# Optimization experiments

Hardware: AMD Instinct MI355X
Metric: run time of the kernel (lower is better)

Reference implementation:

```python
import jax, jax.numpy as jnp
import numpy as np

N, E, IN_F, H, F = 4096, 131072, 512, 8, 32  # n_nodes, n_edges, in_features, n_heads, n_hidden
SLOPE = 0.2


def setup_inputs() -> dict:
    key = jax.random.key(0)
    k1, k2, k3, k4 = jax.random.split(key, 4)
    h = jax.random.normal(k1, (N, IN_F), dtype=jnp.float32)
    edge_index = jax.random.randint(k2, (2, E), 0, N)
    train_mask = jnp.ones((E + N,), dtype=jnp.float32)  # mask values written into adj (incl. self-loops appended in forward)
    W_fc = jax.random.normal(k3, (IN_F, H * F), dtype=jnp.float32) * (1.0 / np.sqrt(IN_F))
    W_attn = jax.random.normal(k4, (2 * F,), dtype=jnp.float32) * (1.0 / np.sqrt(2 * F))
    return {"h": h, "edge_index": edge_index, "train_mask": train_mask, "W_fc": W_fc, "W_attn": W_attn}


def reference(h, edge_index, train_mask, W_fc, W_attn):
    n = h.shape[0]
    g = (h @ W_fc).reshape(n, H, F)  # [n, H, F]
    # attn_fc(concat(g_i, g_j)) == g_i @ W_attn[:F] + g_j @ W_attn[F:]  (same math, no NxNx2F tensor)
    el = g @ W_attn[:F]  # [n, H], contribution of source row i
    er = g @ W_attn[F:]  # [n, H], contribution of column j
    e = jax.nn.leaky_relu(el[:, None, :] + er[None, :, :], SLOPE)  # [n, n, H]
    # adjacency: edges (+ self-loops appended in forward) get train_mask values, then diagonal forced to 1
    src = jnp.concatenate([edge_index[0], jnp.arange(n)])
    dst = jnp.concatenate([edge_index[1], jnp.arange(n)])
    adj = jnp.zeros((n, n), dtype=h.dtype).at[src, dst].set(train_mask)
    diag = jnp.arange(n)
    adj = adj.at[diag, diag].set(1.0)
    e = jnp.where(adj[:, :, None] == 0, -jnp.inf, e)
    a = jax.nn.softmax(e, axis=1)  # softmax over neighbors j (dropout p=0 -> identity)
    attn_res = jnp.einsum('ijh,jhf->ihf', a, g)  # [n, H, F]
    return attn_res.reshape(n, H * F)  # is_concat=True
```

## Files before the change

kernel.cpp:

```cpp
#include <hip/hip_runtime.h>
#include <stdint.h>

#define NN   4096
#define NE   131072
#define KIN  512
#define NH   8
#define HF   256
#define SLOPE 0.2f
#define MAXJ 256

typedef __attribute__((ext_vector_type(8))) short bf16x8;
typedef __attribute__((ext_vector_type(4))) float f32x4;


__device__ __forceinline__ unsigned short f2bf(float x) {
  unsigned u = __builtin_bit_cast(unsigned, x);
  u += 0x7FFFu + ((u >> 16) & 1u);
  return (unsigned short)(u >> 16);
}
__device__ __forceinline__ float bf2f(unsigned short x) {
  unsigned u = ((unsigned)x) << 16;
  return __builtin_bit_cast(float, u);
}
__device__ __forceinline__ unsigned pack2(float lo, float hi) {
  return (unsigned)f2bf(lo) | ((unsigned)f2bf(hi) << 16);
}

__global__ __launch_bounds__(256) void prep_k(const float* __restrict__ B,
                                              unsigned* __restrict__ bitmap,
                                              unsigned short* __restrict__ Btbf) {
  __shared__ float tile[32][33];
  const int b = blockIdx.x, t = threadIdx.x;
  if (b < 512) {
    ((float4*)bitmap)[b * 256 + t] = make_float4(0.f, 0.f, 0.f, 0.f);
  } else {
    int bb = b - 512;
    int k0 = (bb >> 3) * 32, n0 = (bb & 7) * 32;
    int lr = t >> 3, lc = (t & 7) * 4;
    float4 v = *(const float4*)&B[(size_t)(k0 + lr) * HF + n0 + lc];
    tile[lr][lc] = v.x; tile[lr][lc + 1] = v.y; tile[lr][lc + 2] = v.z; tile[lr][lc + 3] = v.w;
    __syncthreads();
    ushort4 o;
    o.x = f2bf(tile[lc + 0][lr]); o.y = f2bf(tile[lc + 1][lr]);
    o.z = f2bf(tile[lc + 2][lr]); o.w = f2bf(tile[lc + 3][lr]);
    *(ushort4*)&Btbf[(size_t)(n0 + lr) * KIN + k0 + lc] = o;
  }
}

__global__ __launch_bounds__(256) void gemm_adj_k(const float* __restrict__ h,
                                                  const unsigned short* __restrict__ Bt,
                                                  const float* __restrict__ Wa,
                                                  unsigned short* __restrict__ gbf,
                                                  float* __restrict__ el,
                                                  float* __restrict__ er,
                                                  const int* __restrict__ ei,
                                                  const float* __restrict__ mask,
                                                  unsigned* __restrict__ bitmap) {
  __shared__ unsigned short smem[2][4096];
  const int bx = blockIdx.x, t = threadIdx.x;
  if (bx >= 1024) {
    int k = (bx - 1024) * 256 + t;
    int s, d; float m;
    if (k < NE) { s = ei[k]; d = ei[NE + k]; m = mask[k]; }
    else        { s = k - NE; d = s; m = 1.0f; }
    if (m != 0.0f) atomicOr(&bitmap[s * 128 + (d >> 5)], 1u << (d & 31));
    return;
  }
  const int gx = bx & 127, gy = bx >> 7;
  const int row0 = gx * 32, col0 = gy * 32;
  const int w = t >> 6, l = t & 63;
  const int wr = w >> 1, wc = w & 1;

  const int srow = (w << 3) + (l >> 3);
  const int sc   = l & 7;
  const int aoff = srow * 64 + ((sc ^ (srow & 7)) << 3);
  const float* gA = &h[(size_t)(row0 + srow) * KIN + sc * 8];
  const int schB = sc ^ (srow & 7);
  const unsigned short* gB = &Bt[(size_t)(col0 + srow) * KIN + schB * 8];

#define BSTAGE(bf, ks)                                                                            \
  __builtin_amdgcn_global_load_lds(                                                               \
      (const __attribute__((address_space(1))) unsigned int*)(gB + (size_t)(ks) * 64),            \
      (__attribute__((address_space(3))) unsigned int*)(&smem[bf][2048 + w * 512]), 16, 0, 0)

  f32x4 acc = {};
  {
    float4 va0 = *(const float4*)(gA);
    float4 va1 = *(const float4*)(gA + 4);
    BSTAGE(0, 0);
    uint4 w4 = {pack2(va0.x, va0.y), pack2(va0.z, va0.w),
                pack2(va1.x, va1.y), pack2(va1.z, va1.w)};
    *(uint4*)&smem[0][aoff] = w4;
  }
  __syncthreads();

  const int lrow = l & 15, kg = l >> 4;
  const int ar = wr * 16 + lrow, br = wc * 16 + lrow;
  for (int ks = 0; ks < 8; ++ks) {
    const int bf = ks & 1;
    float4 na0, na1;
    if (ks < 7) {
      na0 = *(const float4*)(gA + (ks + 1) * 64);
      na1 = *(const float4*)(gA + (ks + 1) * 64 + 4);
      BSTAGE(bf ^ 1, ks + 1);
    }
    bf16x8 a0 = *(const bf16x8*)&smem[bf][ar * 64 + ((kg ^ (ar & 7)) << 3)];
    bf16x8 a1 = *(const bf16x8*)&smem[bf][ar * 64 + (((4 + kg) ^ (ar & 7)) << 3)];
    bf16x8 b0 = *(const bf16x8*)&smem[bf][2048 + br * 64 + ((kg ^ (br & 7)) << 3)];
    bf16x8 b1 = *(const bf16x8*)&smem[bf][2048 + br * 64 + (((4 + kg) ^ (br & 7)) << 3)];
    acc = __builtin_amdgcn_mfma_f32_16x16x32_bf16(a0, b0, acc, 0, 0, 0);
    acc = __builtin_amdgcn_mfma_f32_16x16x32_bf16(a1, b1, acc, 0, 0, 0);
    if (ks < 7) {
      uint4 w4 = {pack2(na0.x, na0.y), pack2(na0.z, na0.w),
                  pack2(na1.x, na1.y), pack2(na1.z, na1.w)};
      *(uint4*)&smem[bf ^ 1][aoff] = w4;
    }
    __syncthreads();
  }
#undef BSTAGE

  const int crow = (l >> 4) * 4, ccol = l & 15;
  const int gr0 = row0 + wr * 16 + crow, gc = col0 + wc * 16 + ccol;
#pragma unroll
  for (int q = 0; q < 4; ++q) gbf[(size_t)(gr0 + q) * HF + gc] = f2bf(acc[q]);

  float* red = (float*)smem;
  const int f = wc * 16 + ccol;
  const float wal = Wa[f], war = Wa[32 + f];
#pragma unroll
  for (int q = 0; q < 4; ++q) {
    float pel = acc[q] * wal, per = acc[q] * war;
#pragma unroll
    for (int m = 8; m >= 1; m >>= 1) { pel += __shfl_xor(pel, m); per += __shfl_xor(per, m); }
    if (ccol == 0) {
      int rl = wr * 16 + crow + q;
      red[wc * 32 + rl] = pel;
      red[64 + wc * 32 + rl] = per;
    }
  }
  __syncthreads();
  if (t < 32) {
    el[(row0 + t) * NH + gy] = red[t] + red[32 + t];
    er[(row0 + t) * NH + gy] = red[64 + t] + red[96 + t];
  }
}

__global__ __launch_bounds__(256) void attn_k(const unsigned* __restrict__ bitmap,
                                              const unsigned short* __restrict__ gbf,
                                              const float* __restrict__ el_,
                                              const float* __restrict__ er_,
                                              float* __restrict__ out) {
  __shared__ unsigned short jl[4][MAXJ];
  const int t = threadIdx.x, wv = t >> 6, l = t & 63;
  const int i = blockIdx.x * 4 + wv;

  unsigned w0 = bitmap[i * 128 + l];
  unsigned w1 = bitmap[i * 128 + 64 + l];
  int cnt = __popc(w0) + __popc(w1);
  int incl = cnt;
#pragma unroll
  for (int d = 1; d < 64; d <<= 1) {
    int u = __shfl_up(incl, d);
    if (l >= d) incl += u;
  }
  int total = __shfl(incl, 63);
  if (total > MAXJ) total = MAXJ;
  int off = incl - cnt;
  unsigned short* J = jl[wv];
  while (w0) {
    int b = __ffs(w0) - 1;
    if (off < MAXJ) J[off] = (unsigned short)(l * 32 + b);
    ++off; w0 &= w0 - 1;
  }
  while (w1) {
    int b = __ffs(w1) - 1;
    if (off < MAXJ) J[off] = (unsigned short)((64 + l) * 32 + b);
    ++off; w1 &= w1 - 1;
  }
  __syncthreads();

  const int hh = l >> 3;
  const float elh = el_[i * NH + hh];
  const unsigned short* gp = gbf + (size_t)l * 4;
  f32x4 accA = {}, accB = {};
  float den0 = 0.f, den1 = 0.f;
  int k = 0;
  for (; k + 4 <= total; k += 4) {
    int j0 = J[k], j1 = J[k + 1], j2 = J[k + 2], j3 = J[k + 3];
    float e0 = elh + er_[j0 * NH + hh];
    float e1 = elh + er_[j1 * NH + hh];
    float e2 = elh + er_[j2 * NH + hh];
    float e3 = elh + er_[j3 * NH + hh];
    ushort4 g0 = *(const ushort4*)(gp + (size_t)j0 * HF);
    ushort4 g1 = *(const ushort4*)(gp + (size_t)j1 * HF);
    ushort4 g2 = *(const ushort4*)(gp + (size_t)j2 * HF);
    ushort4 g3 = *(const ushort4*)(gp + (size_t)j3 * HF);
    float l0 = e0 > 0.f ? e0 : SLOPE * e0;
    float l1 = e1 > 0.f ? e1 : SLOPE * e1;
    float l2 = e2 > 0.f ? e2 : SLOPE * e2;
    float l3 = e3 > 0.f ? e3 : SLOPE * e3;
    float wg0 = __expf(l0), wg1 = __expf(l1), wg2 = __expf(l2), wg3 = __expf(l3);
    den0 += wg0 + wg2; den1 += wg1 + wg3;
    accA[0] += wg0 * bf2f(g0.x); accB[0] += wg1 * bf2f(g1.x);
    accA[1] += wg0 * bf2f(g0.y); accB[1] += wg1 * bf2f(g1.y);
    accA[2] += wg0 * bf2f(g0.z); accB[2] += wg1 * bf2f(g1.z);
    accA[3] += wg0 * bf2f(g0.w); accB[3] += wg1 * bf2f(g1.w);
    accA[0] += wg2 * bf2f(g2.x); accB[0] += wg3 * bf2f(g3.x);
    accA[1] += wg2 * bf2f(g2.y); accB[1] += wg3 * bf2f(g3.y);
    accA[2] += wg2 * bf2f(g2.z); accB[2] += wg3 * bf2f(g3.z);
    accA[3] += wg2 * bf2f(g2.w); accB[3] += wg3 * bf2f(g3.w);
  }
  for (; k < total; ++k) {
    int j0 = J[k];
    float e0 = elh + er_[j0 * NH + hh];
    float l0 = e0 > 0.f ? e0 : SLOPE * e0;
    float wg0 = __expf(l0);
    ushort4 g0 = *(const ushort4*)(gp + (size_t)j0 * HF);
    den0 += wg0;
    accA[0] += wg0 * bf2f(g0.x); accA[1] += wg0 * bf2f(g0.y);
    accA[2] += wg0 * bf2f(g0.z); accA[3] += wg0 * bf2f(g0.w);
  }
  float inv = 1.f / (den0 + den1);
  float4 o = make_float4((accA[0] + accB[0]) * inv, (accA[1] + accB[1]) * inv,
                         (accA[2] + accB[2]) * inv, (accA[3] + accB[3]) * inv);
  *(float4*)&out[(size_t)i * HF + l * 4] = o;
}

extern "C" void kernel_launch(void* const* d_in, const int* in_sizes, int n_in,
                              void* d_out, int out_size, void* d_ws, size_t ws_size,
                              hipStream_t stream) {
  const float* h      = (const float*)d_in[0];
  const int*   ei     = (const int*)d_in[1];
  const float* mask   = (const float*)d_in[2];
  const float* W_fc   = (const float*)d_in[3];
  const float* W_attn = (const float*)d_in[4];
  float* out = (float*)d_out;

  char* ws = (char*)d_ws;
  unsigned* bitmap      = (unsigned*)ws;
  unsigned short* gbf   = (unsigned short*)(ws + (size_t)2 * 1024 * 1024);
  float* el             = (float*)(ws + (size_t)4 * 1024 * 1024);
  float* er             = (float*)(ws + (size_t)4 * 1024 * 1024 + 128 * 1024);
  unsigned short* Btbf  = (unsigned short*)(ws + (size_t)4 * 1024 * 1024 + 256 * 1024);

  prep_k<<<640, 256, 0, stream>>>(W_fc, bitmap, Btbf);
  gemm_adj_k<<<1024 + 528, 256, 0, stream>>>(h, Btbf, W_attn, gbf, el, er, ei, mask, bitmap);
  attn_k<<<NN / 4, 256, 0, stream>>>(bitmap, gbf, el, er, out);
}
```

Baseline: 33.75 us.

## Load GEMM MFMA fragments directly from global memory, dropping LDS staging

```diff
diff --git a/kernel.cpp b/kernel.cpp
--- a/kernel.cpp
+++ b/kernel.cpp
@@ -11,6 +11,7 @@
 
 typedef __attribute__((ext_vector_type(8))) short bf16x8;
 typedef __attribute__((ext_vector_type(4))) float f32x4;
+typedef __attribute__((ext_vector_type(4))) unsigned int u32x4;
 
 
 __device__ __forceinline__ unsigned short f2bf(float x) {
@@ -56,7 +57,7 @@
                                                   const int* __restrict__ ei,
                                                   const float* __restrict__ mask,
                                                   unsigned* __restrict__ bitmap) {
-  __shared__ unsigned short smem[2][4096];
+  __shared__ float red[128];
   const int bx = blockIdx.x, t = threadIdx.x;
   if (bx >= 1024) {
     int k = (bx - 1024) * 256 + t;
@@ -70,61 +71,29 @@
   const int row0 = gx * 32, col0 = gy * 32;
   const int w = t >> 6, l = t & 63;
   const int wr = w >> 1, wc = w & 1;
-
-  const int srow = (w << 3) + (l >> 3);
-  const int sc   = l & 7;
-  const int aoff = srow * 64 + ((sc ^ (srow & 7)) << 3);
-  const float* gA = &h[(size_t)(row0 + srow) * KIN + sc * 8];
-  const int schB = sc ^ (srow & 7);
-  const unsigned short* gB = &Bt[(size_t)(col0 + srow) * KIN + schB * 8];
-
-#define BSTAGE(bf, ks)                                                                            \
-  __builtin_amdgcn_global_load_lds(                                                               \
-      (const __attribute__((address_space(1))) unsigned int*)(gB + (size_t)(ks) * 64),            \
-      (__attribute__((address_space(3))) unsigned int*)(&smem[bf][2048 + w * 512]), 16, 0, 0)
-
-  f32x4 acc = {};
-  {
-    float4 va0 = *(const float4*)(gA);
-    float4 va1 = *(const float4*)(gA + 4);
-    BSTAGE(0, 0);
-    uint4 w4 = {pack2(va0.x, va0.y), pack2(va0.z, va0.w),
-                pack2(va1.x, va1.y), pack2(va1.z, va1.w)};
-    *(uint4*)&smem[0][aoff] = w4;
-  }
-  __syncthreads();
-
   const int lrow = l & 15, kg = l >> 4;
   const int ar = wr * 16 + lrow, br = wc * 16 + lrow;
-  for (int ks = 0; ks < 8; ++ks) {
-    const int bf = ks & 1;
-    float4 na0, na1;
-    if (ks < 7) {
-      na0 = *(const float4*)(gA + (ks + 1) * 64);
-      na1 = *(const float4*)(gA + (ks + 1) * 64 + 4);
-      BSTAGE(bf ^ 1, ks + 1);
-    }
-    bf16x8 a0 = *(const bf16x8*)&smem[bf][ar * 64 + ((kg ^ (ar & 7)) << 3)];
-    bf16x8 a1 = *(const bf16x8*)&smem[bf][ar * 64 + (((4 + kg) ^ (ar & 7)) << 3)];
-    bf16x8 b0 = *(const bf16x8*)&smem[bf][2048 + br * 64 + ((kg ^ (br & 7)) << 3)];
-    bf16x8 b1 = *(const bf16x8*)&smem[bf][2048 + br * 64 + (((4 + kg) ^ (br & 7)) << 3)];
-    acc = __builtin_amdgcn_mfma_f32_16x16x32_bf16(a0, b0, acc, 0, 0, 0);
-    acc = __builtin_amdgcn_mfma_f32_16x16x32_bf16(a1, b1, acc, 0, 0, 0);
-    if (ks < 7) {
-      uint4 w4 = {pack2(na0.x, na0.y), pack2(na0.z, na0.w),
-                  pack2(na1.x, na1.y), pack2(na1.z, na1.w)};
-      *(uint4*)&smem[bf ^ 1][aoff] = w4;
-    }
-    __syncthreads();
-  }
-#undef BSTAGE
+
+  const float* pa = &h[(size_t)(row0 + ar) * KIN + kg * 8];
+  const unsigned short* pb = &Bt[(size_t)(col0 + br) * KIN + kg * 8];
+
+  f32x4 acc = {};
+#pragma unroll 4
+  for (int ks = 0; ks < 16; ++ks) {
+    float4 a0 = *(const float4*)(pa + ks * 32);
+    float4 a1 = *(const float4*)(pa + ks * 32 + 4);
+    bf16x8 bfr = *(const bf16x8*)(pb + ks * 32);
+    u32x4 up = {pack2(a0.x, a0.y), pack2(a0.z, a0.w),
+                pack2(a1.x, a1.y), pack2(a1.z, a1.w)};
+    bf16x8 afr = __builtin_bit_cast(bf16x8, up);
+    acc = __builtin_amdgcn_mfma_f32_16x16x32_bf16(afr, bfr, acc, 0, 0, 0);
+  }
 
   const int crow = (l >> 4) * 4, ccol = l & 15;
   const int gr0 = row0 + wr * 16 + crow, gc = col0 + wc * 16 + ccol;
 #pragma unroll
   for (int q = 0; q < 4; ++q) gbf[(size_t)(gr0 + q) * HF + gc] = f2bf(acc[q]);
 
-  float* red = (float*)smem;
   const int f = wc * 16 + ccol;
   const float wal = Wa[f], war = Wa[32 + f];
 #pragma unroll
```

New measurement: 48.51 us. 1.44x slower.
